# Kernel optimization log

Measured on AMD Instinct MI355X. Metric: run time of the kernel, lower is better.

Reference implementation:

```python
import jax, jax.numpy as jnp
import numpy as np

N = 50000
E = 800000
F_IN = 128


def _gat(h, src, dst, W, a_src, a_dst, bias, heads, out_ch, concat):
    n = h.shape[0]
    z = (h @ W.T).reshape(n, heads, out_ch)              # [N,H,C]
    alpha_s = jnp.sum(z * a_src, axis=-1)                # [N,H]
    alpha_d = jnp.sum(z * a_dst, axis=-1)                # [N,H]
    logits = jax.nn.leaky_relu(alpha_s[src] + alpha_d[dst], 0.2)  # [Etot,H]
    m = jax.ops.segment_max(logits, dst, num_segments=n)
    ex = jnp.exp(logits - m[dst])
    denom = jax.ops.segment_sum(ex, dst, num_segments=n)
    w = ex / (denom[dst] + 1e-16)                        # [Etot,H]
    agg = jax.ops.segment_sum(w[:, :, None] * z[src], dst, num_segments=n)  # [N,H,C]
    if concat:
        out = agg.reshape(n, heads * out_ch)
    else:
        out = agg.mean(axis=1)
    return out + bias


def setup_inputs() -> dict:
    key = jax.random.key(0)
    ks = jax.random.split(key, 16)
    s = lambda *sh: 1.0 / np.sqrt(sh[-1])
    inp = {
        "x": jax.random.normal(ks[0], (N, F_IN), jnp.float32),
        "edge_index": jax.random.randint(ks[1], (2, E), 0, N, jnp.int64),
        # GraphConv(no_node_features=128 -> 128, aggr='add')
        "W_rel": jax.random.normal(ks[2], (128, F_IN), jnp.float32) * s(128, F_IN),
        "b_rel": jnp.zeros((128,), jnp.float32),
        "W_root": jax.random.normal(ks[3], (128, F_IN), jnp.float32) * s(128, F_IN),
        # GATConv(128 -> 8, heads=8, concat) => 64
        "W1": jax.random.normal(ks[4], (64, 128), jnp.float32) * s(64, 128),
        "a1_src": jax.random.normal(ks[5], (8, 8), jnp.float32) * 0.35,
        "a1_dst": jax.random.normal(ks[6], (8, 8), jnp.float32) * 0.35,
        "b1": jnp.zeros((64,), jnp.float32),
        # GATConv(64 -> 64, heads=1, concat=False)
        "W2": jax.random.normal(ks[7], (64, 64), jnp.float32) * s(64, 64),
        "a2_src": jax.random.normal(ks[8], (1, 64), jnp.float32) * 0.125,
        "a2_dst": jax.random.normal(ks[9], (1, 64), jnp.float32) * 0.125,
        "b2": jnp.zeros((64,), jnp.float32),
        "Wr": jax.random.normal(ks[10], (1, 64), jnp.float32) * s(1, 64),
        "br": jnp.zeros((1,), jnp.float32),
    }
    return inp


def reference(x, edge_index, W_rel, b_rel, W_root, W1, a1_src, a1_dst, b1,
              W2, a2_src, a2_dst, b2, Wr, br):
    src, dst = edge_index[0], edge_index[1]
    # GraphConv, aggr='add': W_rel @ sum_{j in N(i)} x_j + b + W_root @ x_i
    nbr = jax.ops.segment_sum(x[src], dst, num_segments=N)
    h = nbr @ W_rel.T + b_rel + x @ W_root.T
    h = jax.nn.elu(h)
    # GATConv adds self-loops by default
    loop = jnp.arange(N, dtype=edge_index.dtype)
    src2 = jnp.concatenate([src, loop])
    dst2 = jnp.concatenate([dst, loop])
    h = _gat(h, src2, dst2, W1, a1_src, a1_dst, b1, heads=8, out_ch=8, concat=True)
    h = jax.nn.elu(h)
    h = _gat(h, src2, dst2, W2, a2_src, a2_dst, b2, heads=1, out_ch=64, concat=False)
    # final 'mean' aggregation over all nodes (single graph)
    g = jnp.mean(h, axis=0, keepdims=True)               # [1,64]
    return g @ Wr.T + br                                  # [1,1]
```

## Files before the change

kernel.cpp:

```cpp
#include <hip/hip_runtime.h>
#include <hip/hip_bf16.h>
#include <math.h>

#define N_NODES 50000
#define N_EDGES 800000
#define F_IN 128
#define NBUCK 391
#define EPB 4096
#define NBB 196

typedef __attribute__((ext_vector_type(8))) short bf16x8;
typedef __attribute__((ext_vector_type(4))) float f32x4;
typedef __attribute__((ext_vector_type(2))) float f32x2;
typedef unsigned long long ull;

__device__ __forceinline__ float elu_f(float x)   { return x > 0.f ? x : expm1f(x); }
__device__ __forceinline__ float lrelu_f(float x) { return x > 0.f ? x : 0.2f * x; }
__device__ __forceinline__ int   clampN(int v)    { return v < 0 ? 0 : (v >= N_NODES ? N_NODES - 1 : v); }
__device__ __forceinline__ float bits2f(unsigned int u) { union { unsigned int u; float f; } x; x.u = u; return x.f; }
__device__ __forceinline__ float bf2f(unsigned short s) { return bits2f(((unsigned int)s) << 16); }
__device__ __forceinline__ unsigned short f2bfbits(float f) {
    __hip_bfloat16 b = __float2bfloat16(f);
    return __builtin_bit_cast(unsigned short, b);
}
__device__ __forceinline__ unsigned int pack2(float lo, float hi) {
    return ((unsigned int)f2bfbits(hi) << 16) | f2bfbits(lo);
}

#define CAST_X_IDS (N_NODES * 32)
#define CAST_IDS (CAST_X_IDS + 32768 + 8192 + 4096)
#define CASTB ((CAST_IDS + 255) / 256)
__global__ __launch_bounds__(256) void k_prep(const int* __restrict__ dst,
                                              const float* __restrict__ x,
                                              const float* __restrict__ W_rel,
                                              const float* __restrict__ W_root,
                                              const float* __restrict__ W1,
                                              const float* __restrict__ W2,
                                              int* __restrict__ part,
                                              __hip_bfloat16* __restrict__ Abuf,
                                              unsigned int* __restrict__ x8,
                                              __hip_bfloat16* __restrict__ Wc,
                                              __hip_bfloat16* __restrict__ W1b,
                                              __hip_bfloat16* __restrict__ W2b,
                                              float* __restrict__ red) {
    __shared__ int hist[NBUCK];
    int tid = threadIdx.x;
    if (blockIdx.x < NBB) {
        for (int j = tid; j < NBUCK; j += 256) hist[j] = 0;
        __syncthreads();
        int base = blockIdx.x * EPB;
        #pragma unroll
        for (int t = 0; t < EPB / 256; ++t) {
            int e = base + t * 256 + tid;
            if (e < N_EDGES) atomicAdd(&hist[clampN(dst[e]) >> 7], 1);
        }
        __syncthreads();
        for (int j = tid; j < NBUCK; j += 256)
            part[(size_t)blockIdx.x * NBUCK + j] = hist[j];
    } else {
        if (blockIdx.x == NBB) red[tid] = 0.f;
        int id = (blockIdx.x - NBB) * 256 + tid;
        if (id < CAST_X_IDS) {
            int i = id >> 5, c4 = (id & 31) * 4;
            float4 v = *(const float4*)&x[(size_t)i * 128 + c4];
            ull p = (ull)f2bfbits(v.x) | ((ull)f2bfbits(v.y) << 16)
                  | ((ull)f2bfbits(v.z) << 32) | ((ull)f2bfbits(v.w) << 48);
            *(ull*)&Abuf[(size_t)i * 256 + 128 + c4] = p;
            int t = __builtin_amdgcn_cvt_pk_fp8_f32(v.x, v.y, 0, false);
            t = __builtin_amdgcn_cvt_pk_fp8_f32(v.z, v.w, t, true);
            x8[(size_t)i * 32 + (id & 31)] = (unsigned int)t;
        } else if (id < CAST_IDS) {
            int j = id - CAST_X_IDS;
            if (j < 32768) {
                int cc = j >> 8, k = j & 255;
                float v = (k < 128) ? W_rel[cc * 128 + k] : W_root[cc * 128 + (k - 128)];
                Wc[j] = __float2bfloat16(v);
            } else if (j < 32768 + 8192) {
                W1b[j - 32768] = __float2bfloat16(W1[j - 32768]);
            } else {
                W2b[j - 32768 - 8192] = __float2bfloat16(W2[j - 32768 - 8192]);
            }
        }
    }
}

__global__ __launch_bounds__(512) void k_bscan(const int* __restrict__ part,
                                               int* __restrict__ boff,
                                               int* __restrict__ bcur) {
    __shared__ int wsum[8];
    __shared__ int wbase[8];
    int tid = threadIdx.x;
    int lane = tid & 63, wid = tid >> 6;
    int v = 0;
    if (tid < NBUCK) {
        for (int b = 0; b < NBB; ++b) v += part[(size_t)b * NBUCK + tid];
    }
    int x = v;
    #pragma unroll
    for (int d = 1; d < 64; d <<= 1) {
        int t = __shfl_up(x, d, 64);
        if (lane >= d) x += t;
    }
    if (lane == 63) wsum[wid] = x;
    __syncthreads();
    if (tid == 0) {
        int b = 0;
        #pragma unroll
        for (int w = 0; w < 8; ++w) { wbase[w] = b; b += wsum[w]; }
    }
    __syncthreads();
    if (tid < NBUCK) {
        int e = wbase[wid] + x - v;
        boff[tid] = e;
        bcur[tid] = e;
    }
    if (tid == 0) boff[NBUCK] = N_EDGES;
}

__global__ __launch_bounds__(256) void k_bscatter(const int* __restrict__ src,
                                                  const int* __restrict__ dst,
                                                  int* __restrict__ bcur,
                                                  unsigned int* __restrict__ ebuf) {
    __shared__ int hist[NBUCK];
    __shared__ int hbase[NBUCK];
    int tid = threadIdx.x;
    for (int j = tid; j < NBUCK; j += 256) hist[j] = 0;
    __syncthreads();
    int base = blockIdx.x * EPB;
    unsigned int myP[EPB / 256]; int myB[EPB / 256], myR[EPB / 256];
    #pragma unroll
    for (int t = 0; t < EPB / 256; ++t) {
        int e = base + t * 256 + tid;
        if (e < N_EDGES) {
            int d = clampN(dst[e]);
            int s = clampN(src[e]);
            myP[t] = ((unsigned int)s << 7) | (unsigned int)(d & 127);
            myB[t] = d >> 7;
            myR[t] = atomicAdd(&hist[d >> 7], 1);
        } else myB[t] = -1;
    }
    __syncthreads();
    for (int j = tid; j < NBUCK; j += 256)
        if (hist[j]) hbase[j] = atomicAdd(&bcur[j], hist[j]);
    __syncthreads();
    #pragma unroll
    for (int t = 0; t < EPB / 256; ++t) {
        if (myB[t] >= 0) ebuf[hbase[myB[t]] + myR[t]] = myP[t];
    }
}

__global__ __launch_bounds__(256) void k_bfinal(const unsigned int* __restrict__ ebuf,
                                                const int* __restrict__ boff,
                                                int* __restrict__ offsets,
                                                int* __restrict__ csr) {
    __shared__ int cnt[128];
    __shared__ int cur[128];
    __shared__ int ws[4];
    int b = blockIdx.x;
    int tid = threadIdx.x;
    int node0 = b << 7;
    int k0 = boff[b], k1 = boff[b + 1];
    if (tid < 128) cnt[tid] = 0;
    __syncthreads();
    for (int k = k0 + tid; k < k1; k += 256)
        atomicAdd(&cnt[ebuf[k] & 127u], 1);
    __syncthreads();
    int lane = tid & 63;
    int v = (tid < 128) ? cnt[tid] : 0;
    int x = v;
    #pragma unroll
    for (int d = 1; d < 64; d <<= 1) {
        int t = __shfl_up(x, d, 64);
        if (lane >= d) x += t;
    }
    if (lane == 63) ws[tid >> 6] = x;
    __syncthreads();
    if (tid < 128) {
        int add = (tid >> 6) ? ws[0] : 0;
        int excl = k0 + add + x - v;
        cur[tid] = excl;
        int node = node0 + tid;
        if (node < N_NODES) offsets[node] = excl;
    }
    if (b == NBUCK - 1 && tid == 0) offsets[N_NODES] = N_EDGES;
    __syncthreads();
    for (int k = k0 + tid; k < k1; k += 256) {
        unsigned int e = ebuf[k];
        int r = atomicAdd(&cur[e & 127u], 1);
        csr[r] = (int)(e >> 7);
    }
}

__global__ __launch_bounds__(256) void k_gather(const unsigned int* __restrict__ x8,
                                                const int* __restrict__ offsets,
                                                const int* __restrict__ csr,
                                                ull* __restrict__ outNbr) {
    int i = blockIdx.x * 8 + (threadIdx.x >> 5);
    int l = threadIdx.x & 31;
    int k0 = offsets[i], k1 = offsets[i + 1];
    float a0 = 0.f, a1 = 0.f, a2 = 0.f, a3 = 0.f;
    for (int kb = k0; kb < k1; kb += 8) {
        int s[8]; int vm[8];
        #pragma unroll
        for (int j = 0; j < 8; ++j) {
            int kk = kb + j;
            vm[j] = kk < k1;
            s[j] = csr[vm[j] ? kk : k1 - 1];
        }
        unsigned int u[8];
        #pragma unroll
        for (int j = 0; j < 8; ++j) u[j] = x8[(size_t)s[j] * 32 + l];
        #pragma unroll
        for (int j = 0; j < 8; ++j) {
            if (vm[j]) {
                f32x2 lo = __builtin_amdgcn_cvt_pk_f32_fp8(u[j], false);
                f32x2 hi = __builtin_amdgcn_cvt_pk_f32_fp8(u[j], true);
                a0 += lo.x; a1 += lo.y; a2 += hi.x; a3 += hi.y;
            }
        }
    }
    outNbr[(size_t)i * 64 + l] = (ull)pack2(a0, a1) | ((ull)pack2(a2, a3) << 32);
}

__global__ __launch_bounds__(256) void k_gemm12(const __hip_bfloat16* __restrict__ A,
                                                const __hip_bfloat16* __restrict__ Wc,
                                                const float* __restrict__ bias,
                                                const __hip_bfloat16* __restrict__ W1b,
                                                const float* __restrict__ a_src,
                                                const float* __restrict__ a_dst,
                                                float* __restrict__ as_o,
                                                float* __restrict__ ad_o,
                                                unsigned int* __restrict__ z8) {
    __shared__ __align__(16) short smem[64 * 136];
    short (*sA)[40] = (short(*)[40])smem;
    short (*sW)[40] = (short(*)[40])(smem + 64 * 40);
    int tid = threadIdx.x;
    int lane = tid & 63, wave = tid >> 6;
    int quad = lane >> 4, l16 = lane & 15;
    int node0 = blockIdx.x * 64;
    int srow = tid >> 2, schk = (tid & 3) * 8;
    int ga = node0 + srow; if (ga >= N_NODES) ga = N_NODES - 1;
    const short* Ap = (const short*)A + (size_t)ga * 256 + schk;
    const short* Wp = (const short*)Wc;
    f32x4 acc[8];
    #pragma unroll
    for (int t = 0; t < 8; ++t) acc[t] = (f32x4){0.f, 0.f, 0.f, 0.f};
    for (int k0 = 0; k0 < 256; k0 += 32) {
        *(bf16x8*)&sA[srow][schk] = *(const bf16x8*)(Ap + k0);
        #pragma unroll
        for (int it = 0; it < 2; ++it) {
            int wrow = srow + it * 64;
            *(bf16x8*)&sW[wrow][schk] = *(const bf16x8*)(Wp + (size_t)wrow * 256 + k0 + schk);
        }
        __syncthreads();
        bf16x8 a = *(const bf16x8*)&sA[wave * 16 + l16][quad * 8];
        #pragma unroll
        for (int nt = 0; nt < 8; ++nt) {
            bf16x8 b = *(const bf16x8*)&sW[nt * 16 + l16][quad * 8];
            acc[nt] = __builtin_amdgcn_mfma_f32_16x16x32_bf16(a, b, acc[nt], 0, 0, 0);
        }
        __syncthreads();
    }
    #pragma unroll
    for (int nt = 0; nt < 8; ++nt) {
        int col = nt * 16 + l16;
        float bv = bias[col];
        #pragma unroll
        for (int r = 0; r < 4; ++r) {
            int row = wave * 16 + quad * 4 + r;
            smem[row * 136 + col] = (short)f2bfbits(elu_f(acc[nt][r] + bv));
        }
    }
    __syncthreads();
    f32x4 acc2[4];
    #pragma unroll
    for (int t = 0; t < 4; ++t) acc2[t] = (f32x4){0.f, 0.f, 0.f, 0.f};
    const short* W1p = (const short*)W1b;
    #pragma unroll
    for (int k0 = 0; k0 < 128; k0 += 32) {
        bf16x8 a = *(const bf16x8*)&smem[(wave * 16 + l16) * 136 + k0 + quad * 8];
        #pragma unroll
        for (int nt = 0; nt < 4; ++nt) {
            bf16x8 b = *(const bf16x8*)(W1p + (size_t)(nt * 16 + l16) * 128 + k0 + quad * 8);
            acc2[nt] = __builtin_amdgcn_mfma_f32_16x16x32_bf16(a, b, acc2[nt], 0, 0, 0);
        }
    }
    __syncthreads();
    #pragma unroll
    for (int nt = 0; nt < 4; ++nt) {
        int col = nt * 16 + l16;
        #pragma unroll
        for (int r = 0; r < 4; ++r) {
            int row = wave * 16 + quad * 4 + r;
            smem[row * 72 + col] = (short)f2bfbits(acc2[nt][r]);
        }
    }
    __syncthreads();
    int row = tid >> 2, chunk = tid & 3;
    int gi = node0 + row;
    float v[16];
    bf16x8 c0 = *(const bf16x8*)&smem[row * 72 + chunk * 16];
    bf16x8 c1 = *(const bf16x8*)&smem[row * 72 + chunk * 16 + 8];
    #pragma unroll
    for (int j = 0; j < 8; ++j) {
        v[j]     = bf2f((unsigned short)c0[j]);
        v[8 + j] = bf2f((unsigned short)c1[j]);
    }
    float ps0 = 0.f, pd0 = 0.f, ps1 = 0.f, pd1 = 0.f;
    #pragma unroll
    for (int j = 0; j < 8; ++j) {
        ps0 += v[j] * a_src[chunk * 16 + j];
        pd0 += v[j] * a_dst[chunk * 16 + j];
        ps1 += v[8 + j] * a_src[chunk * 16 + 8 + j];
        pd1 += v[8 + j] * a_dst[chunk * 16 + 8 + j];
    }
    if (gi < N_NODES) {
        as_o[(size_t)gi * 8 + 2 * chunk]     = ps0;
        as_o[(size_t)gi * 8 + 2 * chunk + 1] = ps1;
        ad_o[(size_t)gi * 8 + 2 * chunk]     = pd0;
        ad_o[(size_t)gi * 8 + 2 * chunk + 1] = pd1;
        #pragma unroll
        for (int wi = 0; wi < 4; ++wi) {
            int t = __builtin_amdgcn_cvt_pk_fp8_f32(v[4 * wi], v[4 * wi + 1], 0, false);
            t = __builtin_amdgcn_cvt_pk_fp8_f32(v[4 * wi + 2], v[4 * wi + 3], t, true);
            z8[(size_t)gi * 16 + chunk * 4 + wi] = (unsigned int)t;
        }
    }
}

__global__ __launch_bounds__(256) void k_gat1z2(const unsigned int* __restrict__ z8,
                                                const float* __restrict__ as1,
                                                const float* __restrict__ ad1,
                                                const float* __restrict__ b1,
                                                const int* __restrict__ offsets,
                                                const int* __restrict__ csr,
                                                const __hip_bfloat16* __restrict__ W2b,
                                                const float* __restrict__ a2s,
                                                const float* __restrict__ a2d,
                                                float* __restrict__ as2,
                                                float* __restrict__ ad2,
                                                unsigned int* __restrict__ z2e8) {
    __shared__ __align__(16) short sH2[16 * 72];
    __shared__ __align__(16) short sZ2[16 * 72];
    int iloc = threadIdx.x >> 4;
    int i = blockIdx.x * 16 + iloc;
    int l = threadIdx.x & 15;
    int hd = l >> 1;
    int wh = l & 7, slot = l >> 3;
    int k0 = offsets[i], k1 = offsets[i + 1];
    float ad_h = ad1[(size_t)i * 8 + hd];
    float adw  = ad1[(size_t)i * 8 + wh];
    float e_self = __expf(lrelu_f(as1[(size_t)i * 8 + hd] + ad_h));
    unsigned int uz = z8[(size_t)i * 16 + l];
    f32x2 zlo = __builtin_amdgcn_cvt_pk_f32_fp8(uz, false);
    f32x2 zhi = __builtin_amdgcn_cvt_pk_f32_fp8(uz, true);
    float acc0 = e_self * zlo.x, acc1 = e_self * zlo.y;
    float acc2 = e_self * zhi.x, acc3 = e_self * zhi.y;
    float denp = 0.f;
    for (int kb = k0; kb < k1; kb += 8) {
        int sr[4]; float er[4];
        #pragma unroll
        for (int m = 0; m < 4; ++m) {
            int kk = kb + 2 * m + slot;
            bool v = kk < k1;
            int s = csr[v ? kk : k1 - 1];
            sr[m] = s;
            er[m] = v ? __expf(lrelu_f(as1[(size_t)s * 8 + wh] + adw)) : 0.f;
            denp += er[m];
        }
        int sj[8]; float ej[8]; unsigned int u[8];
        #pragma unroll
        for (int m = 0; m < 4; ++m) {
            #pragma unroll
            for (int sb = 0; sb < 2; ++sb) {
                sj[2 * m + sb] = __shfl(sr[m], sb * 8 + hd, 16);
                ej[2 * m + sb] = __shfl(er[m], sb * 8 + hd, 16);
            }
        }
        #pragma unroll
        for (int j = 0; j < 8; ++j) u[j] = z8[(size_t)sj[j] * 16 + l];
        #pragma unroll
        for (int j = 0; j < 8; ++j) {
            f32x2 alo = __builtin_amdgcn_cvt_pk_f32_fp8(u[j], false);
            f32x2 ahi = __builtin_amdgcn_cvt_pk_f32_fp8(u[j], true);
            acc0 += ej[j] * alo.x; acc1 += ej[j] * alo.y;
            acc2 += ej[j] * ahi.x; acc3 += ej[j] * ahi.y;
        }
    }
    denp += __shfl_xor(denp, 8, 16);
    float den = __shfl(denp, hd, 16) + e_self;
    float inv = 1.f / den;
    float r0 = elu_f(acc0 * inv + b1[4 * l + 0]);
    float r1 = elu_f(acc1 * inv + b1[4 * l + 1]);
    float r2 = elu_f(acc2 * inv + b1[4 * l + 2]);
    float r3 = elu_f(acc3 * inv + b1[4 * l + 3]);
    *(ull*)&sH2[iloc * 72 + 4 * l] = (ull)pack2(r0, r1) | ((ull)pack2(r2, r3) << 32);
    __syncthreads();
    int lane = threadIdx.x & 63, wave = threadIdx.x >> 6;
    int quad = lane >> 4, l16 = lane & 15;
    f32x4 accz = (f32x4){0.f, 0.f, 0.f, 0.f};
    const short* W2p = (const short*)W2b;
    #pragma unroll
    for (int kk0 = 0; kk0 < 64; kk0 += 32) {
        bf16x8 a = *(const bf16x8*)&sH2[l16 * 72 + kk0 + quad * 8];
        bf16x8 b = *(const bf16x8*)(W2p + (size_t)(wave * 16 + l16) * 64 + kk0 + quad * 8);
        accz = __builtin_amdgcn_mfma_f32_16x16x32_bf16(a, b, accz, 0, 0, 0);
    }
    #pragma unroll
    for (int r = 0; r < 4; ++r)
        sZ2[(quad * 4 + r) * 72 + wave * 16 + l16] = (short)f2bfbits(accz[r]);
    __syncthreads();
    ull pz = *(const ull*)&sZ2[iloc * 72 + 4 * l];
    float v0 = bf2f((unsigned short)(pz & 0xffff));
    float v1 = bf2f((unsigned short)((pz >> 16) & 0xffff));
    float v2 = bf2f((unsigned short)((pz >> 32) & 0xffff));
    float v3 = bf2f((unsigned short)(pz >> 48));
    float ps = v0 * a2s[4 * l + 0] + v1 * a2s[4 * l + 1] + v2 * a2s[4 * l + 2] + v3 * a2s[4 * l + 3];
    float pd = v0 * a2d[4 * l + 0] + v1 * a2d[4 * l + 1] + v2 * a2d[4 * l + 2] + v3 * a2d[4 * l + 3];
    #pragma unroll
    for (int d = 8; d >= 1; d >>= 1) {
        ps += __shfl_xor(ps, d, 16);
        pd += __shfl_xor(pd, d, 16);
    }
    if (l == 0) { as2[i] = ps; ad2[i] = pd; }
    int t = __builtin_amdgcn_cvt_pk_fp8_f32(v0, v1, 0, false);
    t = __builtin_amdgcn_cvt_pk_fp8_f32(v2, v3, t, true);
    z2e8[(size_t)i * 16 + l] = (unsigned int)t;
}

__global__ __launch_bounds__(256) void k_gat2attn(const unsigned int* __restrict__ z8,
                                                  const float* __restrict__ as2,
                                                  const float* __restrict__ ad2,
                                                  const float* __restrict__ b2,
                                                  const int* __restrict__ offsets,
                                                  const int* __restrict__ csr,
                                                  const float* __restrict__ Wr,
                                                  float* __restrict__ red) {
    int i = blockIdx.x * 16 + (threadIdx.x >> 4);
    int l = threadIdx.x & 15;
    int k0 = offsets[i], k1 = offsets[i + 1];
    float ad = ad2[i];
    float e_self = __expf(lrelu_f(as2[i] + ad));
    unsigned int uz = z8[(size_t)i * 16 + l];
    f32x2 zlo = __builtin_amdgcn_cvt_pk_f32_fp8(uz, false);
    f32x2 zhi = __builtin_amdgcn_cvt_pk_f32_fp8(uz, true);
    float acc0 = e_self * zlo.x, acc1 = e_self * zlo.y;
    float acc2 = e_self * zhi.x, acc3 = e_self * zhi.y;
    float denp = (l == 0) ? e_self : 0.f;
    for (int kb = k0; kb < k1; kb += 16) {
        int kk = kb + l;
        bool v = kk < k1;
        int s = csr[v ? kk : k1 - 1];
        float e = v ? __expf(lrelu_f(as2[s] + ad)) : 0.f;
        denp += e;
        int nv = k1 - kb; if (nv > 16) nv = 16;
        for (int j0 = 0; j0 < nv; j0 += 8) {
            int sj[8]; float ej[8]; unsigned int u[8];
            #pragma unroll
            for (int j = 0; j < 8; ++j) {
                int idx = (j0 + j) & 15;
                sj[j] = __shfl(s, idx, 16);
                ej[j] = __shfl(e, idx, 16);
            }
            #pragma unroll
            for (int j = 0; j < 8; ++j) u[j] = z8[(size_t)sj[j] * 16 + l];
            #pragma unroll
            for (int j = 0; j < 8; ++j) {
                f32x2 alo = __builtin_amdgcn_cvt_pk_f32_fp8(u[j], false);
                f32x2 ahi = __builtin_amdgcn_cvt_pk_f32_fp8(u[j], true);
                acc0 += ej[j] * alo.x; acc1 += ej[j] * alo.y;
                acc2 += ej[j] * ahi.x; acc3 += ej[j] * ahi.y;
            }
        }
    }
    #pragma unroll
    for (int d = 8; d >= 1; d >>= 1) denp += __shfl_xor(denp, d, 16);
    float inv = 1.f / denp;
    float c = (acc0 * inv + b2[4 * l + 0]) * Wr[4 * l + 0]
            + (acc1 * inv + b2[4 * l + 1]) * Wr[4 * l + 1]
            + (acc2 * inv + b2[4 * l + 2]) * Wr[4 * l + 2]
            + (acc3 * inv + b2[4 * l + 3]) * Wr[4 * l + 3];
    #pragma unroll
    for (int d = 8; d >= 1; d >>= 1) c += __shfl_xor(c, d, 64);
    if (l == 0) atomicAdd(&red[blockIdx.x & 255], c);
}

__global__ void k_finalize(const float* __restrict__ red, const float* __restrict__ br,
                           float* __restrict__ out) {
    int t = threadIdx.x;
    float s = red[t] + red[t + 64] + red[t + 128] + red[t + 192];
    #pragma unroll
    for (int d = 32; d >= 1; d >>= 1) s += __shfl_xor(s, d, 64);
    if (t == 0) out[0] = s * (1.0f / N_NODES) + br[0];
}

extern "C" void kernel_launch(void* const* d_in, const int* in_sizes, int n_in,
                              void* d_out, int out_size, void* d_ws, size_t ws_size,
                              hipStream_t stream) {
    const float* x      = (const float*)d_in[0];
    const int*   edges  = (const int*)d_in[1];
    const float* W_rel  = (const float*)d_in[2];
    const float* b_rel  = (const float*)d_in[3];
    const float* W_root = (const float*)d_in[4];
    const float* W1     = (const float*)d_in[5];
    const float* a1s    = (const float*)d_in[6];
    const float* a1d    = (const float*)d_in[7];
    const float* b1     = (const float*)d_in[8];
    const float* W2     = (const float*)d_in[9];
    const float* a2s    = (const float*)d_in[10];
    const float* a2d    = (const float*)d_in[11];
    const float* b2     = (const float*)d_in[12];
    const float* Wr     = (const float*)d_in[13];
    const float* br     = (const float*)d_in[14];
    float* out = (float*)d_out;

    const int* src = edges;
    const int* dst = edges + N_EDGES;

    char* ws = (char*)d_ws;
    size_t p = 0;
    auto alloc = [&](size_t bytes) -> void* {
        void* r = ws + p;
        p = (p + bytes + 255) & ~(size_t)255;
        return r;
    };
    int*   part    = (int*)alloc((size_t)NBB * NBUCK * 4);
    int*   boff    = (int*)alloc((size_t)(NBUCK + 1) * 4);
    int*   bcur    = (int*)alloc((size_t)NBUCK * 4);
    unsigned int* ebuf = (unsigned int*)alloc((size_t)N_EDGES * 4);
    int*   offsets = (int*)alloc((size_t)(N_NODES + 1) * 4);
    int*   csr     = (int*)alloc((size_t)N_EDGES * 4);
    __hip_bfloat16* Abuf = (__hip_bfloat16*)alloc((size_t)N_NODES * 256 * 2);
    unsigned int* x8 = (unsigned int*)alloc((size_t)N_NODES * 32 * 4);
    __hip_bfloat16* Wc   = (__hip_bfloat16*)alloc((size_t)128 * 256 * 2);
    __hip_bfloat16* W1b  = (__hip_bfloat16*)alloc((size_t)64 * 128 * 2);
    __hip_bfloat16* W2b  = (__hip_bfloat16*)alloc((size_t)64 * 64 * 2);
    float* as1 = (float*)alloc((size_t)N_NODES * 8 * 4);
    float* ad1 = (float*)alloc((size_t)N_NODES * 8 * 4);
    float* as2 = (float*)alloc((size_t)N_NODES * 4);
    float* ad2 = (float*)alloc((size_t)N_NODES * 4);
    unsigned int* z1e8 = (unsigned int*)alloc((size_t)N_NODES * 16 * 4);
    unsigned int* z2e8 = (unsigned int*)alloc((size_t)N_NODES * 16 * 4);
    float* red = (float*)alloc(256 * 4);

    const int MB   = (N_NODES + 63) / 64;
    const int NB8  = N_NODES / 8;
    const int NB16 = N_NODES / 16;

    k_prep    <<<NBB + CASTB, 256, 0, stream>>>(dst, x, W_rel, W_root, W1, W2,
                                                part, Abuf, x8, Wc, W1b, W2b, red);
    k_bscan   <<<1, 512, 0, stream>>>(part, boff, bcur);
    k_bscatter<<<NBB, 256, 0, stream>>>(src, dst, bcur, ebuf);
    k_bfinal  <<<NBUCK, 256, 0, stream>>>(ebuf, boff, offsets, csr);
    k_gather  <<<NB8, 256, 0, stream>>>(x8, offsets, csr, (ull*)Abuf);
    k_gemm12  <<<MB, 256, 0, stream>>>(Abuf, Wc, b_rel, W1b, a1s, a1d, as1, ad1, z1e8);
    k_gat1z2  <<<NB16, 256, 0, stream>>>(z1e8, as1, ad1, b1, offsets, csr,
                                         W2b, a2s, a2d, as2, ad2, z2e8);
    k_gat2attn<<<NB16, 256, 0, stream>>>(z2e8, as2, ad2, b2, offsets, csr, Wr, red);
    k_finalize<<<1, 64, 0, stream>>>(red, br, out);
}
```

Before: 241.6 us.

## Project GAT2 features onto regression weight before aggregation; fuse finalize via last-block

Because the final readout is linear, each node's 64-dim layer-2 feature is projected onto Wr in k_gat1z2, giving one scalar per node. The layer-2 attention kernel then aggregates scalars instead of gathering 64-channel fp8 rows, which removes most of the gather traffic. The separate finalize launch is folded into the attention kernel with a done-counter last-block reduction. The bias term is handled as b2·Wr, which is exact because the attention weights sum to one. This adds a counter that must be reset each call.

```diff
diff --git a/kernel.cpp b/kernel.cpp
--- a/kernel.cpp
+++ b/kernel.cpp
@@ -42,7 +42,8 @@
                                               __hip_bfloat16* __restrict__ Wc,
                                               __hip_bfloat16* __restrict__ W1b,
                                               __hip_bfloat16* __restrict__ W2b,
-                                              float* __restrict__ red) {
+                                              float* __restrict__ red,
+                                              int* __restrict__ done) {
     __shared__ int hist[NBUCK];
     int tid = threadIdx.x;
     if (blockIdx.x < NBB) {
@@ -58,7 +59,10 @@
         for (int j = tid; j < NBUCK; j += 256)
             part[(size_t)blockIdx.x * NBUCK + j] = hist[j];
     } else {
-        if (blockIdx.x == NBB) red[tid] = 0.f;
+        if (blockIdx.x == NBB) {
+            red[tid] = 0.f;
+            if (tid == 0) done[0] = 0;
+        }
         int id = (blockIdx.x - NBB) * 256 + tid;
         if (id < CAST_X_IDS) {
             int i = id >> 5, c4 = (id & 31) * 4;
@@ -337,9 +341,10 @@
                                                 const __hip_bfloat16* __restrict__ W2b,
                                                 const float* __restrict__ a2s,
                                                 const float* __restrict__ a2d,
+                                                const float* __restrict__ Wr,
                                                 float* __restrict__ as2,
                                                 float* __restrict__ ad2,
-                                                unsigned int* __restrict__ z2e8) {
+                                                float* __restrict__ zr) {
     __shared__ __align__(16) short sH2[16 * 72];
     __shared__ __align__(16) short sZ2[16 * 72];
     int iloc = threadIdx.x >> 4;
@@ -417,81 +422,76 @@
     float v3 = bf2f((unsigned short)(pz >> 48));
     float ps = v0 * a2s[4 * l + 0] + v1 * a2s[4 * l + 1] + v2 * a2s[4 * l + 2] + v3 * a2s[4 * l + 3];
     float pd = v0 * a2d[4 * l + 0] + v1 * a2d[4 * l + 1] + v2 * a2d[4 * l + 2] + v3 * a2d[4 * l + 3];
+    float pr = v0 * Wr[4 * l + 0]  + v1 * Wr[4 * l + 1]  + v2 * Wr[4 * l + 2]  + v3 * Wr[4 * l + 3];
     #pragma unroll
     for (int d = 8; d >= 1; d >>= 1) {
         ps += __shfl_xor(ps, d, 16);
         pd += __shfl_xor(pd, d, 16);
-    }
-    if (l == 0) { as2[i] = ps; ad2[i] = pd; }
-    int t = __builtin_amdgcn_cvt_pk_fp8_f32(v0, v1, 0, false);
-    t = __builtin_amdgcn_cvt_pk_fp8_f32(v2, v3, t, true);
-    z2e8[(size_t)i * 16 + l] = (unsigned int)t;
-}
-
-__global__ __launch_bounds__(256) void k_gat2attn(const unsigned int* __restrict__ z8,
-                                                  const float* __restrict__ as2,
-                                                  const float* __restrict__ ad2,
-                                                  const float* __restrict__ b2,
-                                                  const int* __restrict__ offsets,
-                                                  const int* __restrict__ csr,
-                                                  const float* __restrict__ Wr,
-                                                  float* __restrict__ red) {
-    int i = blockIdx.x * 16 + (threadIdx.x >> 4);
-    int l = threadIdx.x & 15;
-    int k0 = offsets[i], k1 = offsets[i + 1];
-    float ad = ad2[i];
-    float e_self = __expf(lrelu_f(as2[i] + ad));
-    unsigned int uz = z8[(size_t)i * 16 + l];
-    f32x2 zlo = __builtin_amdgcn_cvt_pk_f32_fp8(uz, false);
-    f32x2 zhi = __builtin_amdgcn_cvt_pk_f32_fp8(uz, true);
-    float acc0 = e_self * zlo.x, acc1 = e_self * zlo.y;
-    float acc2 = e_self * zhi.x, acc3 = e_self * zhi.y;
-    float denp = (l == 0) ? e_self : 0.f;
-    for (int kb = k0; kb < k1; kb += 16) {
-        int kk = kb + l;
-        bool v = kk < k1;
-        int s = csr[v ? kk : k1 - 1];
-        float e = v ? __expf(lrelu_f(as2[s] + ad)) : 0.f;
-        denp += e;
-        int nv = k1 - kb; if (nv > 16) nv = 16;
-        for (int j0 = 0; j0 < nv; j0 += 8) {
-            int sj[8]; float ej[8]; unsigned int u[8];
+        pr += __shfl_xor(pr, d, 16);
+    }
+    if (l == 0) { as2[i] = ps; ad2[i] = pd; zr[i] = pr; }
+}
+
+__global__ __launch_bounds__(256) void k_gat2s(const float* __restrict__ zr,
+                                               const float* __restrict__ as2,
+                                               const float* __restrict__ ad2,
+                                               const int* __restrict__ offsets,
+                                               const int* __restrict__ csr,
+                                               const float* __restrict__ b2,
+                                               const float* __restrict__ Wr,
+                                               const float* __restrict__ br,
+                                               float* __restrict__ red,
+                                               int* __restrict__ done,
+                                               float* __restrict__ out) {
+    __shared__ float wsum[4];
+    __shared__ int lastFlag;
+    int tid = threadIdx.x;
+    int n = blockIdx.x * 64 + (tid >> 2);
+    int r = tid & 3;
+    float c = 0.f;
+    if (n < N_NODES) {
+        int k0 = offsets[n], k1 = offsets[n + 1];
+        float ad = ad2[n];
+        float den = 0.f, num = 0.f;
+        for (int k = k0 + r; k < k1; k += 4) {
+            int s = csr[k];
+            float e = __expf(lrelu_f(as2[s] + ad));
+            den += e;
+            num += e * zr[s];
+        }
+        den += __shfl_xor(den, 1, 64); den += __shfl_xor(den, 2, 64);
+        num += __shfl_xor(num, 1, 64); num += __shfl_xor(num, 2, 64);
+        if (r == 0) {
+            float es = __expf(lrelu_f(as2[n] + ad));
+            den += es;
+            num += es * zr[n];
+            c = num / den;
+        }
+    }
+    #pragma unroll
+    for (int d = 4; d <= 32; d <<= 1) c += __shfl_xor(c, d, 64);
+    int lane = tid & 63, wave = tid >> 6;
+    if (lane == 0) wsum[wave] = c;
+    __syncthreads();
+    if (tid == 0) {
+        float s = wsum[0] + wsum[1] + wsum[2] + wsum[3];
+        atomicAdd(&red[blockIdx.x & 255], s);
+        __threadfence();
+        int old = atomicAdd(done, 1);
+        lastFlag = (old == (int)gridDim.x - 1);
+    }
+    __syncthreads();
+    if (lastFlag) {
+        __threadfence();
+        if (tid < 64) {
+            float rv = atomicAdd(&red[tid], 0.f) + atomicAdd(&red[tid + 64], 0.f)
+                     + atomicAdd(&red[tid + 128], 0.f) + atomicAdd(&red[tid + 192], 0.f);
+            float p = rv * (1.0f / N_NODES) + b2[tid] * Wr[tid];
             #pragma unroll
-            for (int j = 0; j < 8; ++j) {
-                int idx = (j0 + j) & 15;
-                sj[j] = __shfl(s, idx, 16);
-                ej[j] = __shfl(e, idx, 16);
-            }
-            #pragma unroll
-            for (int j = 0; j < 8; ++j) u[j] = z8[(size_t)sj[j] * 16 + l];
-            #pragma unroll
-            for (int j = 0; j < 8; ++j) {
-                f32x2 alo = __builtin_amdgcn_cvt_pk_f32_fp8(u[j], false);
-                f32x2 ahi = __builtin_amdgcn_cvt_pk_f32_fp8(u[j], true);
-                acc0 += ej[j] * alo.x; acc1 += ej[j] * alo.y;
-                acc2 += ej[j] * ahi.x; acc3 += ej[j] * ahi.y;
-            }
-        }
-    }
-    #pragma unroll
-    for (int d = 8; d >= 1; d >>= 1) denp += __shfl_xor(denp, d, 16);
-    float inv = 1.f / denp;
-    float c = (acc0 * inv + b2[4 * l + 0]) * Wr[4 * l + 0]
-            + (acc1 * inv + b2[4 * l + 1]) * Wr[4 * l + 1]
-            + (acc2 * inv + b2[4 * l + 2]) * Wr[4 * l + 2]
-            + (acc3 * inv + b2[4 * l + 3]) * Wr[4 * l + 3];
-    #pragma unroll
-    for (int d = 8; d >= 1; d >>= 1) c += __shfl_xor(c, d, 64);
-    if (l == 0) atomicAdd(&red[blockIdx.x & 255], c);
-}
-
-__global__ void k_finalize(const float* __restrict__ red, const float* __restrict__ br,
-                           float* __restrict__ out) {
-    int t = threadIdx.x;
-    float s = red[t] + red[t + 64] + red[t + 128] + red[t + 192];
-    #pragma unroll
-    for (int d = 32; d >= 1; d >>= 1) s += __shfl_xor(s, d, 64);
-    if (t == 0) out[0] = s * (1.0f / N_NODES) + br[0];
+            for (int d = 32; d >= 1; d >>= 1) p += __shfl_xor(p, d, 64);
+            if (tid == 0) out[0] = p + br[0];
+        }
+    }
 }
 
 extern "C" void kernel_launch(void* const* d_in, const int* in_sizes, int n_in,
@@ -539,23 +539,24 @@
     float* ad1 = (float*)alloc((size_t)N_NODES * 8 * 4);
     float* as2 = (float*)alloc((size_t)N_NODES * 4);
     float* ad2 = (float*)alloc((size_t)N_NODES * 4);
+    float* zr  = (float*)alloc((size_t)N_NODES * 4);
     unsigned int* z1e8 = (unsigned int*)alloc((size_t)N_NODES * 16 * 4);
-    unsigned int* z2e8 = (unsigned int*)alloc((size_t)N_NODES * 16 * 4);
     float* red = (float*)alloc(256 * 4);
+    int*   done = (int*)alloc(4);
 
     const int MB   = (N_NODES + 63) / 64;
     const int NB8  = N_NODES / 8;
     const int NB16 = N_NODES / 16;
 
     k_prep    <<<NBB + CASTB, 256, 0, stream>>>(dst, x, W_rel, W_root, W1, W2,
-                                                part, Abuf, x8, Wc, W1b, W2b, red);
+                                                part, Abuf, x8, Wc, W1b, W2b, red, done);
     k_bscan   <<<1, 512, 0, stream>>>(part, boff, bcur);
     k_bscatter<<<NBB, 256, 0, stream>>>(src, dst, bcur, ebuf);
     k_bfinal  <<<NBUCK, 256, 0, stream>>>(ebuf, boff, offsets, csr);
     k_gather  <<<NB8, 256, 0, stream>>>(x8, offsets, csr, (ull*)Abuf);
     k_gemm12  <<<MB, 256, 0, stream>>>(Abuf, Wc, b_rel, W1b, a1s, a1d, as1, ad1, z1e8);
     k_gat1z2  <<<NB16, 256, 0, stream>>>(z1e8, as1, ad1, b1, offsets, csr,
-                                         W2b, a2s, a2d, as2, ad2, z2e8);
-    k_gat2attn<<<NB16, 256, 0, stream>>>(z2e8, as2, ad2, b2, offsets, csr, Wr, red);
-    k_finalize<<<1, 64, 0, stream>>>(red, br, out);
-}
+                                         W2b, a2s, a2d, Wr, as2, ad2, zr);
+    k_gat2s   <<<MB, 256, 0, stream>>>(zr, as2, ad2, offsets, csr, b2, Wr, br,
+                                       red, done, out);
+}
```

Result: faster. 235.8 us (-2.4%).
